# Kernel optimization log

Hardware: AMD Instinct MI355X
Metric: run time of the kernel (lower is better)

## Reference

```python
import jax, jax.numpy as jnp
import numpy as np

NUM_USERS = 100_000
NUM_ITEMS = 50_000
VEC_DIM = 64
NUM_LAYERS = 3
NUM_INTER = 2_000_000
N_NODES = NUM_USERS + NUM_ITEMS


def setup_inputs() -> dict:
    rng = np.random.default_rng(0)
    u = rng.integers(0, NUM_USERS, NUM_INTER)
    i = rng.integers(0, NUM_ITEMS, NUM_INTER)
    # dok_matrix assignment dedupes repeated (u,i) pairs -> unique edges
    pairs = np.unique(np.stack([u, i], axis=1), axis=0)
    u = pairs[:, 0]
    i = pairs[:, 1] + NUM_USERS  # item nodes offset by num_users
    # symmetric bipartite adjacency in COO form
    rows = np.concatenate([u, i]).astype(np.int32)
    cols = np.concatenate([i, u]).astype(np.int32)
    # D^-1/2 A D^-1/2 normalization (0 where degree == 0)
    deg = np.bincount(rows, minlength=N_NODES).astype(np.float32)
    dinv = np.where(deg > 0, deg ** -0.5, 0.0).astype(np.float32)
    vals = (dinv[rows] * dinv[cols]).astype(np.float32)

    key = jax.random.key(0)
    k_emb, k_usr = jax.random.split(key)
    embed_weights = 0.1 * jax.random.normal(k_emb, (N_NODES, VEC_DIM), dtype=jnp.float32)
    user_idxs = jax.random.randint(k_usr, (8192,), 0, NUM_USERS, dtype=jnp.int64)
    return {
        "embed_weights": embed_weights,
        "vals": jnp.asarray(vals),
        "user_idxs": user_idxs,
        "rows": jnp.asarray(rows),
        "cols": jnp.asarray(cols),
    }


def reference(embed_weights, vals, user_idxs, rows, cols):
    # Faithful to the source: every layer applies the SpMM to the ORIGINAL
    # embedding weights (the torch code never reassigns embed_weights).
    acc = embed_weights  # layer-0 embedding
    for _ in range(NUM_LAYERS):
        # y[r] = sum_e vals[e] * E[cols[e]]  (sparse A @ E)
        layer = jax.ops.segment_sum(
            vals[:, None] * embed_weights[cols], rows, num_segments=N_NODES
        )
        acc = acc + layer
    mean_embed = acc / jnp.float32(NUM_LAYERS + 1)
    user_embed = mean_embed[:NUM_USERS]
    item_embed = mean_embed[NUM_USERS:]
    return user_embed, item_embed
```

## Files before the change

kernel.cpp:

```cpp
#include <hip/hip_runtime.h>
#include <cmath>


constexpr int VEC_DIM   = 64;
constexpr int NUM_USERS = 100000;
constexpr int NGRP      = 8;

__global__ void user_rowptr_kernel(const int* __restrict__ rows,
                                   int* __restrict__ row_ptr_u, int half) {
    int e = blockIdx.x * blockDim.x + threadIdx.x;
    if (e >= half) return;
    int r0 = rows[e];
    int r1 = (e + 1 < half) ? rows[e + 1] : NUM_USERS;
    if (e == 0) {
        for (int r = 0; r <= r0; ++r) row_ptr_u[r] = 0;
    }
    for (int r = r0 + 1; r <= r1; ++r) row_ptr_u[r] = e + 1;
}

__global__ void hist8_kernel(const int* __restrict__ cols,
                             int* __restrict__ H, int half, int chunk, int NI) {
    int b = blockIdx.x;
    int g = b & 7, w = b >> 3;
    int el = w * 256 + threadIdx.x;
    if (el >= chunk) return;
    int e = g * chunk + el;
    if (e >= half) return;
    atomicAdd(&H[g * NI + (cols[e] - NUM_USERS)], 1);
}

__global__ void block_sum_kernel(const int* __restrict__ cnt,
                                 int* __restrict__ blk_sum, int n) {
    __shared__ int s[256];
    const int t = threadIdx.x;
    const int i = blockIdx.x * 256 + t;
    s[t] = (i < n) ? cnt[i] : 0;
    __syncthreads();
    for (int off = 128; off > 0; off >>= 1) {
        if (t < off) s[t] += s[t + off];
        __syncthreads();
    }
    if (t == 0) blk_sum[blockIdx.x] = s[0];
}

__global__ void __launch_bounds__(1024)
blk_scan_kernel(const int* __restrict__ blk_sum, int* __restrict__ blk_off,
                int* __restrict__ total_out, int nblk) {
    __shared__ int s[1024];
    const int t = threadIdx.x;
    const int v = (t < nblk) ? blk_sum[t] : 0;
    s[t] = v;
    __syncthreads();
    for (int off = 1; off < 1024; off <<= 1) {
        int u = (t >= off) ? s[t - off] : 0;
        __syncthreads();
        s[t] += u;
        __syncthreads();
    }
    if (t < nblk) blk_off[t] = s[t] - v;
    if (t == nblk - 1) *total_out = s[t];
}

__global__ void scan_finalize_kernel(const int* __restrict__ cnt,
                                     const int* __restrict__ blk_off,
                                     int* __restrict__ row_ptr,
                                     int* __restrict__ cursor, int n) {
    __shared__ int s[256];
    const int t = threadIdx.x;
    const int i = blockIdx.x * 256 + t;
    const int v = (i < n) ? cnt[i] : 0;
    s[t] = v;
    __syncthreads();
    for (int off = 1; off < 256; off <<= 1) {
        int u = (t >= off) ? s[t - off] : 0;
        __syncthreads();
        s[t] += u;
        __syncthreads();
    }
    if (i < n) {
        int excl = s[t] - v + blk_off[blockIdx.x];
        row_ptr[i] = excl;
        cursor[i]  = excl;
    }
}

__global__ void dinv_kernel(const int* __restrict__ row_ptr_u,
                            const int* __restrict__ H,
                            float* __restrict__ dinv, int n_rows, int NI) {
    int n = blockIdx.x * blockDim.x + threadIdx.x;
    if (n >= n_rows) return;
    int deg;
    if (n < NUM_USERS) {
        deg = row_ptr_u[n + 1] - row_ptr_u[n];
    } else {
        int it = n - NUM_USERS;
        deg = 0;
        #pragma unroll
        for (int g = 0; g < NGRP; ++g) deg += H[g * NI + it];
    }
    dinv[n] = (deg > 0) ? (1.0f / sqrtf((float)deg)) : 0.0f;
}

__global__ void scatter8_kernel(const int* __restrict__ rows,
                                const int* __restrict__ cols,
                                int* __restrict__ cursor,
                                int* __restrict__ csr_u,
                                int half, int chunk, int NI) {
    int b = blockIdx.x;
    int g = b & 7, w = b >> 3;
    int el = w * 256 + threadIdx.x;
    if (el >= chunk) return;
    int e = g * chunk + el;
    if (e >= half) return;
    int slot = atomicAdd(&cursor[g * NI + (cols[e] - NUM_USERS)], 1);
    csr_u[slot] = rows[e];
}

__global__ void __launch_bounds__(256)
gather_kernel(const float* __restrict__ emb,
              const int* __restrict__ row_ptr_u,
              const int* __restrict__ cols,
              const int* __restrict__ S,
              const int* __restrict__ csr_u,
              const float* __restrict__ dinv,
              float* __restrict__ out, int n_rows, int NI) {
    const int wave = threadIdx.x >> 6;
    const int lane = threadIdx.x & 63;
    const int row  = blockIdx.x * 4 + wave;
    if (row >= n_rows) return;

    float acc = 0.0f;
    if (row < NUM_USERS) {
        const int beg = row_ptr_u[row], end = row_ptr_u[row + 1];
        for (int base = beg; base < end; base += 64) {
            const int cnt = min(64, end - base);
            int   c  = cols[base + min(lane, cnt - 1)];
            float dv = dinv[c];
            #pragma unroll 4
            for (int k = 0; k < cnt; ++k) {
                int   ck = __shfl(c, k);
                float vk = __shfl(dv, k);
                acc += vk * emb[(size_t)ck * VEC_DIM + lane];
            }
        }
    } else {
        const int it = row - NUM_USERS;
        for (int g = 0; g < NGRP; ++g) {
            const int x  = g * NI + it;
            const int s1 = S[x + 1];
            for (int base = S[x]; base < s1; base += 64) {
                const int cnt = min(64, s1 - base);
                int   u  = csr_u[base + min(lane, cnt - 1)];
                float dv = dinv[u];
                #pragma unroll 4
                for (int k = 0; k < cnt; ++k) {
                    int   uk = __shfl(u, k);
                    float vk = __shfl(dv, k);
                    acc += vk * emb[(size_t)uk * VEC_DIM + lane];
                }
            }
        }
    }

    const size_t o = (size_t)row * VEC_DIM + lane;
    out[o] = 0.25f * emb[o] + 0.75f * dinv[row] * acc;
}

__global__ void init_out_kernel(const float4* __restrict__ emb,
                                float4* __restrict__ out, int n4) {
    int i = blockIdx.x * blockDim.x + threadIdx.x;
    if (i < n4) {
        float4 e = emb[i];
        out[i] = make_float4(0.25f * e.x, 0.25f * e.y, 0.25f * e.z, 0.25f * e.w);
    }
}

__global__ void spmm_atomic_kernel(const float* __restrict__ emb,
                                   const float* __restrict__ vals,
                                   const int* __restrict__ rows,
                                   const int* __restrict__ cols,
                                   float* __restrict__ out, int nnz) {
    int tid = blockIdx.x * blockDim.x + threadIdx.x;
    int e = tid >> 4;
    if (e >= nnz) return;
    int d4 = (tid & 15) << 2;
    float v = 0.75f * vals[e];
    int r = rows[e];
    int c = cols[e];
    const float4 ev = *reinterpret_cast<const float4*>(emb + (size_t)c * VEC_DIM + d4);
    float* dst = out + (size_t)r * VEC_DIM + d4;
    atomicAdd(dst + 0, v * ev.x);
    atomicAdd(dst + 1, v * ev.y);
    atomicAdd(dst + 2, v * ev.z);
    atomicAdd(dst + 3, v * ev.w);
}

extern "C" void kernel_launch(void* const* d_in, const int* in_sizes, int n_in,
                              void* d_out, int out_size, void* d_ws, size_t ws_size,
                              hipStream_t stream) {
    const float* emb  = (const float*)d_in[0];
    const float* vals = (const float*)d_in[1];
    const int* rows   = (const int*)d_in[3];
    const int* cols   = (const int*)d_in[4];
    float* out        = (float*)d_out;

    const int nnz    = in_sizes[1];
    const int half   = nnz / 2;
    const int n_rows = out_size / VEC_DIM;
    const int NI     = n_rows - NUM_USERS;
    const int NH     = NGRP * NI;
    const int nb0    = (NH + 255) / 256;
    const int nb1    = (nb0 + 255) / 256;
    const int chunk  = (half + NGRP - 1) / NGRP;
    const int nbpg   = (chunk + 255) / 256;

    const size_t need = ((size_t)NUM_USERS + 1 + 3 * (size_t)NH + 1
                         + 2 * (size_t)nb0 + 2 * (size_t)nb1
                         + (size_t)n_rows + (size_t)half) * 4;

    if (ws_size >= need && NI > 0 && nb1 <= 1024) {
        int* row_ptr_u = (int*)d_ws;
        int* H         = row_ptr_u + NUM_USERS + 1;
        int* S         = H + NH;
        int* cursor    = S + NH + 1;
        int* s1        = cursor + NH;
        int* s1_off    = s1 + nb0;
        int* s2        = s1_off + nb0;
        int* s2_off    = s2 + nb1;
        float* dinv    = (float*)(s2_off + nb1);
        int* csr_u     = (int*)(dinv + n_rows);

        hipMemsetAsync(H, 0, (size_t)NH * 4, stream);
        user_rowptr_kernel<<<(half + 255) / 256, 256, 0, stream>>>(
            rows, row_ptr_u, half);
        hist8_kernel<<<nbpg * NGRP, 256, 0, stream>>>(cols, H, half, chunk, NI);
        block_sum_kernel<<<nb0, 256, 0, stream>>>(H, s1, NH);
        block_sum_kernel<<<nb1, 256, 0, stream>>>(s1, s2, nb0);
        blk_scan_kernel<<<1, 1024, 0, stream>>>(s2, s2_off, S + NH, nb1);
        scan_finalize_kernel<<<nb1, 256, 0, stream>>>(s1, s2_off,
                                                      s1_off, s1_off, nb0);
        scan_finalize_kernel<<<nb0, 256, 0, stream>>>(H, s1_off, S, cursor, NH);
        dinv_kernel<<<(n_rows + 255) / 256, 256, 0, stream>>>(
            row_ptr_u, H, dinv, n_rows, NI);
        scatter8_kernel<<<nbpg * NGRP, 256, 0, stream>>>(
            rows, cols, cursor, csr_u, half, chunk, NI);
        gather_kernel<<<(n_rows + 3) / 4, 256, 0, stream>>>(
            emb, row_ptr_u, cols, S, csr_u, dinv, out, n_rows, NI);
    } else {
        const int n4 = out_size / 4;
        init_out_kernel<<<(n4 + 255) / 256, 256, 0, stream>>>(
            (const float4*)emb, (float4*)out, n4);
        long long total = (long long)nnz * 16;
        spmm_atomic_kernel<<<(int)((total + 255) / 256), 256, 0, stream>>>(
            emb, vals, rows, cols, out, nnz);
    }
}
```

Baseline: 559.5 us.

## Fuse row-pointer build into histogram pass and unroll gather with independent accumulators

Result: faster. 497.8 us (-11.0%).

```diff
diff --git a/kernel.cpp b/kernel.cpp
--- a/kernel.cpp
+++ b/kernel.cpp
@@ -1,32 +1,30 @@
 #include <hip/hip_runtime.h>
-#include <cmath>
 
 
 constexpr int VEC_DIM   = 64;
 constexpr int NUM_USERS = 100000;
 constexpr int NGRP      = 8;
 
-__global__ void user_rowptr_kernel(const int* __restrict__ rows,
-                                   int* __restrict__ row_ptr_u, int half) {
-    int e = blockIdx.x * blockDim.x + threadIdx.x;
-    if (e >= half) return;
-    int r0 = rows[e];
-    int r1 = (e + 1 < half) ? rows[e + 1] : NUM_USERS;
-    if (e == 0) {
-        for (int r = 0; r <= r0; ++r) row_ptr_u[r] = 0;
-    }
-    for (int r = r0 + 1; r <= r1; ++r) row_ptr_u[r] = e + 1;
-}
-
-__global__ void hist8_kernel(const int* __restrict__ cols,
-                             int* __restrict__ H, int half, int chunk, int NI) {
+__global__ void build_pass1_kernel(const int* __restrict__ rows,
+                                   const int* __restrict__ cols,
+                                   int* __restrict__ row_ptr_u,
+                                   int* __restrict__ H,
+                                   int half, int chunk, int NI) {
     int b = blockIdx.x;
     int g = b & 7, w = b >> 3;
     int el = w * 256 + threadIdx.x;
     if (el >= chunk) return;
     int e = g * chunk + el;
     if (e >= half) return;
+
     atomicAdd(&H[g * NI + (cols[e] - NUM_USERS)], 1);
+
+    int r0 = rows[e];
+    int r1 = (e + 1 < half) ? rows[e + 1] : NUM_USERS;
+    if (e == 0) {
+        for (int r = 0; r <= r0; ++r) row_ptr_u[r] = 0;
+    }
+    for (int r = r0 + 1; r <= r1; ++r) row_ptr_u[r] = e + 1;
 }
 
 __global__ void block_sum_kernel(const int* __restrict__ cnt,
@@ -120,6 +118,7 @@
 gather_kernel(const float* __restrict__ emb,
               const int* __restrict__ row_ptr_u,
               const int* __restrict__ cols,
+              const float* __restrict__ vals,
               const int* __restrict__ S,
               const int* __restrict__ csr_u,
               const float* __restrict__ dinv,
@@ -129,41 +128,51 @@
     const int row  = blockIdx.x * 4 + wave;
     if (row >= n_rows) return;
 
-    float acc = 0.0f;
+    float a0 = 0.0f, a1 = 0.0f, a2 = 0.0f, a3 = 0.0f;
+    float acc;
+
     if (row < NUM_USERS) {
         const int beg = row_ptr_u[row], end = row_ptr_u[row + 1];
-        for (int base = beg; base < end; base += 64) {
-            const int cnt = min(64, end - base);
-            int   c  = cols[base + min(lane, cnt - 1)];
-            float dv = dinv[c];
-            #pragma unroll 4
-            for (int k = 0; k < cnt; ++k) {
-                int   ck = __shfl(c, k);
-                float vk = __shfl(dv, k);
-                acc += vk * emb[(size_t)ck * VEC_DIM + lane];
-            }
+        int e = beg;
+        for (; e + 3 < end; e += 4) {
+            int   c0 = cols[e],     c1 = cols[e + 1];
+            int   c2 = cols[e + 2], c3 = cols[e + 3];
+            float v0 = vals[e],     v1 = vals[e + 1];
+            float v2 = vals[e + 2], v3 = vals[e + 3];
+            a0 += v0 * emb[(size_t)c0 * VEC_DIM + lane];
+            a1 += v1 * emb[(size_t)c1 * VEC_DIM + lane];
+            a2 += v2 * emb[(size_t)c2 * VEC_DIM + lane];
+            a3 += v3 * emb[(size_t)c3 * VEC_DIM + lane];
         }
+        for (; e < end; ++e)
+            a0 += vals[e] * emb[(size_t)cols[e] * VEC_DIM + lane];
+        acc = (a0 + a1) + (a2 + a3);
     } else {
         const int it = row - NUM_USERS;
         for (int g = 0; g < NGRP; ++g) {
             const int x  = g * NI + it;
+            int e        = S[x];
             const int s1 = S[x + 1];
-            for (int base = S[x]; base < s1; base += 64) {
-                const int cnt = min(64, s1 - base);
-                int   u  = csr_u[base + min(lane, cnt - 1)];
-                float dv = dinv[u];
-                #pragma unroll 4
-                for (int k = 0; k < cnt; ++k) {
-                    int   uk = __shfl(u, k);
-                    float vk = __shfl(dv, k);
-                    acc += vk * emb[(size_t)uk * VEC_DIM + lane];
-                }
+            for (; e + 3 < s1; e += 4) {
+                int u0 = csr_u[e],     u1 = csr_u[e + 1];
+                int u2 = csr_u[e + 2], u3 = csr_u[e + 3];
+                float d0 = dinv[u0], d1 = dinv[u1];
+                float d2 = dinv[u2], d3 = dinv[u3];
+                a0 += d0 * emb[(size_t)u0 * VEC_DIM + lane];
+                a1 += d1 * emb[(size_t)u1 * VEC_DIM + lane];
+                a2 += d2 * emb[(size_t)u2 * VEC_DIM + lane];
+                a3 += d3 * emb[(size_t)u3 * VEC_DIM + lane];
+            }
+            for (; e < s1; ++e) {
+                int u = csr_u[e];
+                a0 += dinv[u] * emb[(size_t)u * VEC_DIM + lane];
             }
         }
+        acc = dinv[row] * ((a0 + a1) + (a2 + a3));
     }
 
     const size_t o = (size_t)row * VEC_DIM + lane;
-    out[o] = 0.25f * emb[o] + 0.75f * dinv[row] * acc;
+    out[o] = 0.25f * emb[o] + 0.75f * acc;
 }
 
 __global__ void init_out_kernel(const float4* __restrict__ emb,
@@ -231,9 +240,8 @@
         int* csr_u     = (int*)(dinv + n_rows);
 
         hipMemsetAsync(H, 0, (size_t)NH * 4, stream);
-        user_rowptr_kernel<<<(half + 255) / 256, 256, 0, stream>>>(
-            rows, row_ptr_u, half);
-        hist8_kernel<<<nbpg * NGRP, 256, 0, stream>>>(cols, H, half, chunk, NI);
+        build_pass1_kernel<<<nbpg * NGRP, 256, 0, stream>>>(
+            rows, cols, row_ptr_u, H, half, chunk, NI);
         block_sum_kernel<<<nb0, 256, 0, stream>>>(H, s1, NH);
         block_sum_kernel<<<nb1, 256, 0, stream>>>(s1, s2, nb0);
         blk_scan_kernel<<<1, 1024, 0, stream>>>(s2, s2_off, S + NH, nb1);
@@ -245,7 +253,7 @@
         scatter8_kernel<<<nbpg * NGRP, 256, 0, stream>>>(
             rows, cols, cursor, csr_u, half, chunk, NI);
         gather_kernel<<<(n_rows + 3) / 4, 256, 0, stream>>>(
-            emb, row_ptr_u, cols, S, csr_u, dinv, out, n_rows, NI);
+            emb, row_ptr_u, cols, vals, S, csr_u, dinv, out, n_rows, NI);
     } else {
         const int n4 = out_size / 4;
         init_out_kernel<<<(n4 + 255) / 256, 256, 0, stream>>>(
```
